# Kernel optimization log

Hardware: AMD Instinct MI355X
Metric: run time of the kernel (lower is better)

The kernel has to match this reference:

```python
import jax, jax.numpy as jnp
import numpy as np

B, L, K, E, D, H = 16, 512, 48, 128, 384, 128

def _gelu(x):
    return jax.nn.gelu(x, approximate=False)  # torch nn.GELU default is erf-based

def setup_inputs() -> dict:
    key = jax.random.key(0)
    ks = jax.random.split(key, 16)
    def randn(k, shape, scale=1.0):
        return jax.random.normal(k, shape, dtype=jnp.float32) * scale
    inp = {
        "h_V": randn(ks[0], (B, L, D)),
        "h_E": randn(ks[1], (B, L, K, E)),
        "mask": jnp.ones((B, L), dtype=jnp.float32),
        "fw1": randn(ks[2], (E, D), 1.0 / np.sqrt(E)),
        "fb1": randn(ks[3], (D,), 0.02),
        "fw2": randn(ks[4], (D, D), 1.0 / np.sqrt(D)),
        "fb2": randn(ks[5], (D,), 0.02),
        "hw1": randn(ks[6], (D, H), 1.0 / np.sqrt(D)),
        "hb1": randn(ks[7], (H,), 0.02),
        "hw2": randn(ks[8], (H, H // 2), 1.0 / np.sqrt(H)),
        "hb2": randn(ks[9], (H // 2,), 0.02),
        "hw3": randn(ks[10], (H // 2, 1), 1.0 / np.sqrt(H // 2)),
        "hb3": randn(ks[11], (1,), 0.02),
        "E_idx": jax.random.randint(ks[12], (B, L, K), 0, L),
    }
    return inp

def reference(h_V, h_E, mask, fw1, fb1, fw2, fb2, hw1, hb1, hw2, hb2, hw3, hb3, E_idx):
    # CFConv: edge-conditioned filters [B,L,K,D]
    W = _gelu(_gelu(h_E @ fw1 + fb1) @ fw2 + fb2)
    # gather_nodes: x_j[b,l,k,:] = h_V[b, E_idx[b,l,k], :]
    x_j = jax.vmap(lambda x, idx: x[idx])(h_V, E_idx)  # [B,L,K,D]
    h = jnp.sum(x_j * W, axis=2)  # weighted sum over neighbors -> [B,L,D]
    # mlp_head (dropout = identity at inference)
    h = _gelu(h @ hw1 + hb1)
    h = _gelu(h @ hw2 + hb2)
    dG = (h @ hw3 + hb3)[..., 0]  # [B,L]
    valid_length = jnp.clip(jnp.sum(mask, axis=1), 1.0, None)  # [B]
    return jnp.sum(dG * mask, axis=1) / jnp.sqrt(valid_length)  # [B]
```

## Files before the change

### kernel.cpp

```cpp
#include <hip/hip_runtime.h>
#include <hip/hip_bf16.h>
#include <math.h>

#define NB 16
#define NL 512
#define NK 48
#define NE 128
#define ND 384
#define NH 128

typedef __attribute__((ext_vector_type(8))) short short8;
typedef __attribute__((ext_vector_type(4))) float f32x4;

__device__ __forceinline__ float gelu_fast(float x) {
    float t = x * fmaf(x * x, -0.1029437f, -2.3022087f);
    float e = __builtin_amdgcn_exp2f(t);
    return x * __builtin_amdgcn_rcpf(1.0f + e);
}

__device__ __forceinline__ unsigned short f2bf(float x) {
    union { float f; unsigned u; } v; v.f = x;
    unsigned r = v.u + 0x7fffu + ((v.u >> 16) & 1u);
    return (unsigned short)(r >> 16);
}

__device__ __forceinline__ unsigned short f2bf_rhu(float x) {
    union { float f; unsigned u; } v; v.f = x;
    return (unsigned short)((v.u + 0x8000u) >> 16);
}

__device__ __forceinline__ unsigned pk_bf16(float a, float b) {
    union { float f; unsigned u; } ua, ub; ua.f = a; ub.f = b;
    return __builtin_amdgcn_perm(ua.u + 0x8000u, ub.u + 0x8000u, 0x07060302u);
}

__global__ void pack_weights(const float* __restrict__ fw1,
                             const float* __restrict__ fw2,
                             const float* __restrict__ hw1,
                             const float* __restrict__ hw2,
                             unsigned short* __restrict__ fw1p,
                             unsigned short* __restrict__ fw2p,
                             unsigned short* __restrict__ hw1p,
                             unsigned short* __restrict__ hw2p) {
    int tid = blockIdx.x * 256 + threadIdx.x;
    if (tid < NE * ND) {
        int k = tid / ND, n = tid % ND;
        int dst = (((k >> 5) * 24 + (n >> 4)) * 64 + ((k >> 3) & 3) * 16 + (n & 15)) * 8 + (k & 7);
        fw1p[dst] = f2bf(fw1[tid]);
    } else if (tid < NE * ND + ND * ND) {
        int i = tid - NE * ND;
        int k = i / ND, n = i % ND;
        int dst = (((k >> 5) * 24 + (n >> 4)) * 64 + ((k >> 3) & 3) * 16 + (n & 15)) * 8 + (k & 7);
        fw2p[dst] = f2bf(fw2[i]);
    } else if (tid < NE * ND + ND * ND + ND * NH) {
        int i = tid - (NE * ND + ND * ND);
        int k = i / NH, n = i % NH;
        int dst = (((k >> 5) * 8 + (n >> 4)) * 64 + ((k >> 3) & 3) * 16 + (n & 15)) * 8 + (k & 7);
        hw1p[dst] = f2bf(hw1[i]);
    } else if (tid < NE * ND + ND * ND + ND * NH + NH * (NH / 2)) {
        int i = tid - (NE * ND + ND * ND + ND * NH);
        int k = i / (NH / 2), n = i % (NH / 2);
        int dst = (((k >> 5) * 4 + (n >> 4)) * 64 + ((k >> 3) & 3) * 16 + (n & 15)) * 8 + (k & 7);
        hw2p[dst] = f2bf(hw2[i]);
    }
}

__global__ __launch_bounds__(256, 3) void cfconv_kernel(
    const float* __restrict__ h_V, const float* __restrict__ h_E,
    const float* __restrict__ fb1, const float* __restrict__ fb2,
    const unsigned short* __restrict__ fw1p,
    const unsigned short* __restrict__ fw2p,
    const int* __restrict__ E_idx, unsigned short* __restrict__ hbufB)
{
    __shared__ unsigned short Ea[48 * 136];
    __shared__ unsigned short T[48 * 392];
    __shared__ int rowoff_s[48];

    const int t = threadIdx.x;
    const int wave = t >> 6, lane = t & 63;
    const int quad = lane >> 4, l16 = lane & 15;
    const int bl = blockIdx.x;
    const int wn0 = wave * 96;

    if (t < 48)
        rowoff_s[t] = ((bl >> 9) * NL + E_idx[bl * NK + t]) * ND;

    {
        const float4* src = (const float4*)(h_E + (size_t)bl * (NK * NE));
        #pragma unroll
        for (int i = 0; i < 6; i++) {
            int v = i * 256 + t;
            float4 d = src[v];
            int r = v >> 5;
            int c = (v & 31) * 4;
            uint2 u;
            u.x = pk_bf16(d.y, d.x);
            u.y = pk_bf16(d.w, d.z);
            *(uint2*)&Ea[r * 136 + c] = u;
        }
    }
    __syncthreads();

    f32x4 acc[18];

    #pragma unroll
    for (int i = 0; i < 18; i++) acc[i] = (f32x4){0.f, 0.f, 0.f, 0.f};

    #pragma unroll
    for (int kt = 0; kt < 4; kt++) {
        short8 aw[6], be[3];
        #pragma unroll
        for (int mt = 0; mt < 6; mt++)
            aw[mt] = *(const short8*)(fw1p + (size_t)((kt * 24 + (wn0 >> 4) + mt) * 64 + lane) * 8);
        #pragma unroll
        for (int nt = 0; nt < 3; nt++)
            be[nt] = *(const short8*)&Ea[(nt * 16 + l16) * 136 + kt * 32 + quad * 8];
        #pragma unroll
        for (int mt = 0; mt < 6; mt++)
            #pragma unroll
            for (int nt = 0; nt < 3; nt++)
                acc[mt * 3 + nt] = __builtin_amdgcn_mfma_f32_16x16x32_bf16(
                    aw[mt], be[nt], acc[mt * 3 + nt], 0, 0, 0);
    }

    #pragma unroll
    for (int mt = 0; mt < 6; mt++) {
        float4 b1v = *(const float4*)&fb1[wn0 + mt * 16 + quad * 4];
        #pragma unroll
        for (int nt = 0; nt < 3; nt++) {
            f32x4 a = acc[mt * 3 + nt];
            float v0 = gelu_fast(a[0] + b1v.x);
            float v1 = gelu_fast(a[1] + b1v.y);
            float v2 = gelu_fast(a[2] + b1v.z);
            float v3 = gelu_fast(a[3] + b1v.w);
            uint2 u;
            u.x = pk_bf16(v1, v0);
            u.y = pk_bf16(v3, v2);
            *(uint2*)&T[(nt * 16 + l16) * 392 + wn0 + mt * 16 + quad * 4] = u;
        }
    }
    __syncthreads();

    #pragma unroll
    for (int i = 0; i < 18; i++) acc[i] = (f32x4){0.f, 0.f, 0.f, 0.f};

    {
        short8 b0[6], b1[6], af[3];
        #define LOADB(kt, bf)                                                            \
            _Pragma("unroll")                                                            \
            for (int nt = 0; nt < 6; nt++)                                               \
                bf[nt] = *(const short8*)(fw2p +                                         \
                    (size_t)(((kt) * 24 + (wn0 >> 4) + nt) * 64 + lane) * 8);
        #define LOADA(kt)                                                                \
            _Pragma("unroll")                                                            \
            for (int mt = 0; mt < 3; mt++)                                               \
                af[mt] = *(const short8*)&T[(mt * 16 + l16) * 392 + (kt) * 32 + quad * 8];
        #define MFMAS(bf)                                                                \
            _Pragma("unroll")                                                            \
            for (int mt = 0; mt < 3; mt++)                                               \
                _Pragma("unroll")                                                        \
                for (int nt = 0; nt < 6; nt++)                                           \
                    acc[nt * 3 + mt] = __builtin_amdgcn_mfma_f32_16x16x32_bf16(          \
                        af[mt], bf[nt], acc[nt * 3 + mt], 0, 0, 0);

        LOADB(0, b0);
        for (int kt = 0; kt < 10; kt += 2) {
            LOADB(kt + 1, b1);
            LOADA(kt);
            MFMAS(b0);
            LOADB(kt + 2, b0);
            LOADA(kt + 1);
            MFMAS(b1);
        }
        LOADB(11, b1);
        LOADA(10);
        MFMAS(b0);
        LOADA(11);
        MFMAS(b1);
        #undef LOADB
        #undef LOADA
        #undef MFMAS
    }

    float b2v[6];
    #pragma unroll
    for (int nt = 0; nt < 6; nt++) b2v[nt] = fb2[wn0 + nt * 16 + l16];

    float s[6] = {0.f, 0.f, 0.f, 0.f, 0.f, 0.f};
    #pragma unroll
    for (int mt = 0; mt < 3; mt++) {
        const int rb = mt * 16 + quad * 4;
        const float* p0 = h_V + rowoff_s[rb + 0] + wn0 + l16;
        const float* p1 = h_V + rowoff_s[rb + 1] + wn0 + l16;
        const float* p2 = h_V + rowoff_s[rb + 2] + wn0 + l16;
        const float* p3 = h_V + rowoff_s[rb + 3] + wn0 + l16;
        float xv[6][4];
        #pragma unroll
        for (int nt = 0; nt < 6; nt++) {
            xv[nt][0] = p0[nt * 16];
            xv[nt][1] = p1[nt * 16];
            xv[nt][2] = p2[nt * 16];
            xv[nt][3] = p3[nt * 16];
        }
        #pragma unroll
        for (int nt = 0; nt < 6; nt++)
            #pragma unroll
            for (int r = 0; r < 4; r++)
                s[nt] = fmaf(gelu_fast(acc[nt * 3 + mt][r] + b2v[nt]), xv[nt][r], s[nt]);
    }
    #pragma unroll
    for (int nt = 0; nt < 6; nt++) {
        float v = s[nt];
        v += __shfl_xor(v, 16, 64);
        v += __shfl_xor(v, 32, 64);
        if (lane < 16)
            hbufB[(size_t)bl * ND + wn0 + nt * 16 + lane] = f2bf(v);
    }
}

__global__ __launch_bounds__(64) void head_kernel(
    const unsigned short* __restrict__ hbufB,
    const unsigned short* __restrict__ hw1p, const float* __restrict__ hb1,
    const unsigned short* __restrict__ hw2p, const float* __restrict__ hb2,
    const float* __restrict__ hw3, const float* __restrict__ hb3,
    const float* __restrict__ mask, float* __restrict__ dGpart)
{
    __shared__ unsigned short T1[16 * 136];
    const int lane = threadIdx.x;
    const int quad = lane >> 4, l16 = lane & 15;
    const int row0 = blockIdx.x * 16;

    f32x4 acc1[8];
    #pragma unroll
    for (int nt = 0; nt < 8; nt++) acc1[nt] = (f32x4){0.f, 0.f, 0.f, 0.f};

    for (int kt = 0; kt < 12; kt++) {
        short8 a = *(const short8*)(hbufB + (size_t)(row0 + l16) * ND + kt * 32 + quad * 8);
        #pragma unroll
        for (int nt = 0; nt < 8; nt++) {
            short8 b = *(const short8*)(hw1p + (size_t)((kt * 8 + nt) * 64 + lane) * 8);
            acc1[nt] = __builtin_amdgcn_mfma_f32_16x16x32_bf16(a, b, acc1[nt], 0, 0, 0);
        }
    }

    #pragma unroll
    for (int nt = 0; nt < 8; nt++) {
        int col = nt * 16 + l16;
        float b1 = hb1[col];
        #pragma unroll
        for (int r = 0; r < 4; r++)
            T1[(quad * 4 + r) * 136 + col] = f2bf_rhu(gelu_fast(acc1[nt][r] + b1));
    }
    __syncthreads();

    f32x4 acc2[4];
    #pragma unroll
    for (int nt = 0; nt < 4; nt++) acc2[nt] = (f32x4){0.f, 0.f, 0.f, 0.f};

    #pragma unroll
    for (int kt = 0; kt < 4; kt++) {
        short8 a = *(const short8*)&T1[l16 * 136 + kt * 32 + quad * 8];
        #pragma unroll
        for (int nt = 0; nt < 4; nt++) {
            short8 b = *(const short8*)(hw2p + (size_t)((kt * 4 + nt) * 64 + lane) * 8);
            acc2[nt] = __builtin_amdgcn_mfma_f32_16x16x32_bf16(a, b, acc2[nt], 0, 0, 0);
        }
    }

    float w3[4], b2[4];
    #pragma unroll
    for (int nt = 0; nt < 4; nt++) { w3[nt] = hw3[nt * 16 + l16]; b2[nt] = hb2[nt * 16 + l16]; }

    float dsum = 0.f;
    const float hb3v = hb3[0];
    #pragma unroll
    for (int r = 0; r < 4; r++) {
        float pr = 0.f;
        #pragma unroll
        for (int nt = 0; nt < 4; nt++)
            pr = fmaf(gelu_fast(acc2[nt][r] + b2[nt]), w3[nt], pr);
        pr += __shfl_xor(pr, 1, 64);
        pr += __shfl_xor(pr, 2, 64);
        pr += __shfl_xor(pr, 4, 64);
        pr += __shfl_xor(pr, 8, 64);
        if (l16 == 0) {
            int grow = row0 + quad * 4 + r;
            dsum = fmaf(pr + hb3v, mask[grow], dsum);
        }
    }
    dsum += __shfl_xor(dsum, 16, 64);
    dsum += __shfl_xor(dsum, 32, 64);
    if (lane == 0) dGpart[blockIdx.x] = dsum;
}

__global__ void finalize_kernel(const float* __restrict__ dGpart,
                                const float* __restrict__ mask,
                                float* __restrict__ out) {
    int t = threadIdx.x;
    int b = t >> 4, j = t & 15;
    float ms = 0.f;
    for (int l = j; l < NL; l += 16) ms += mask[b * NL + l];
    float dg = dGpart[b * 32 + j] + dGpart[b * 32 + 16 + j];
    #pragma unroll
    for (int d = 1; d < 16; d <<= 1) {
        ms += __shfl_xor(ms, d, 64);
        dg += __shfl_xor(dg, d, 64);
    }
    if (j == 0) {
        ms = fmaxf(ms, 1.0f);
        out[b] = dg / sqrtf(ms);
    }
}

extern "C" void kernel_launch(void* const* d_in, const int* in_sizes, int n_in,
                              void* d_out, int out_size, void* d_ws, size_t ws_size,
                              hipStream_t stream) {
    const float* h_V  = (const float*)d_in[0];
    const float* h_E  = (const float*)d_in[1];
    const float* mask = (const float*)d_in[2];
    const float* fw1  = (const float*)d_in[3];
    const float* fb1  = (const float*)d_in[4];
    const float* fw2  = (const float*)d_in[5];
    const float* fb2  = (const float*)d_in[6];
    const float* hw1  = (const float*)d_in[7];
    const float* hb1  = (const float*)d_in[8];
    const float* hw2  = (const float*)d_in[9];
    const float* hb2  = (const float*)d_in[10];
    const float* hw3  = (const float*)d_in[11];
    const float* hb3  = (const float*)d_in[12];
    const int*   E_idx = (const int*)d_in[13];
    float* out = (float*)d_out;

    char* ws = (char*)d_ws;
    unsigned short* fw1p = (unsigned short*)ws;
    unsigned short* fw2p = (unsigned short*)(ws + 98304);
    unsigned short* hw1p = (unsigned short*)(ws + 393216);
    unsigned short* hw2p = (unsigned short*)(ws + 491520);
    float* dGpart = (float*)(ws + 507904);
    unsigned short* hbufB = (unsigned short*)(ws + 512000);

    pack_weights<<<992, 256, 0, stream>>>(fw1, fw2, hw1, hw2, fw1p, fw2p, hw1p, hw2p);
    cfconv_kernel<<<NB * NL, 256, 0, stream>>>(h_V, h_E, fb1, fb2, fw1p, fw2p, E_idx, hbufB);
    head_kernel<<<(NB * NL) / 16, 64, 0, stream>>>(hbufB, hw1p, hb1, hw2p, hb2, hw3, hb3, mask, dGpart);
    finalize_kernel<<<1, 256, 0, stream>>>(dGpart, mask, out);
}
```

Before: 453.8 us.

## Process four nodes per block with register prefetch of next node's edges

Each block of the CFConv kernel now loops over four consecutive (b,l) nodes instead of one. The next node's h_E tile and neighbor indices are loaded into registers while the current node's two GEMMs run, then written to shared memory at the end of the iteration. The second GEMM is split into two 48-column passes so fewer accumulators are live, which offsets the extra prefetch registers. The aim is to hide global load latency and amortize block launch cost. In exchange the grid has four times fewer blocks, which reduces parallelism across CUs, and extra barriers are added per node.

```diff
diff --git a/kernel.cpp b/kernel.cpp
--- a/kernel.cpp
+++ b/kernel.cpp
@@ -8,6 +8,7 @@
 #define NE 128
 #define ND 384
 #define NH 128
+#define GRP 4
 
 typedef __attribute__((ext_vector_type(8))) short short8;
 typedef __attribute__((ext_vector_type(4))) float f32x4;
@@ -74,147 +75,179 @@
 {
     __shared__ unsigned short Ea[48 * 136];
     __shared__ unsigned short T[48 * 392];
-    __shared__ int rowoff_s[48];
+    __shared__ int rowoff_s[2][48];
 
     const int t = threadIdx.x;
     const int wave = t >> 6, lane = t & 63;
     const int quad = lane >> 4, l16 = lane & 15;
-    const int bl = blockIdx.x;
+    const int bl0 = blockIdx.x * GRP;
     const int wn0 = wave * 96;
 
-    if (t < 48)
-        rowoff_s[t] = ((bl >> 9) * NL + E_idx[bl * NK + t]) * ND;
-
+    float4 st[6];
     {
-        const float4* src = (const float4*)(h_E + (size_t)bl * (NK * NE));
+        const float4* src = (const float4*)(h_E + (size_t)bl0 * (NK * NE));
+        #pragma unroll
+        for (int i = 0; i < 6; i++) st[i] = src[i * 256 + t];
+        if (t < 48)
+            rowoff_s[0][t] = ((bl0 >> 9) * NL + E_idx[bl0 * NK + t]) * ND;
         #pragma unroll
         for (int i = 0; i < 6; i++) {
             int v = i * 256 + t;
-            float4 d = src[v];
-            int r = v >> 5;
-            int c = (v & 31) * 4;
+            int r = v >> 5, c = (v & 31) * 4;
             uint2 u;
-            u.x = pk_bf16(d.y, d.x);
-            u.y = pk_bf16(d.w, d.z);
+            u.x = pk_bf16(st[i].y, st[i].x);
+            u.y = pk_bf16(st[i].w, st[i].z);
             *(uint2*)&Ea[r * 136 + c] = u;
         }
     }
     __syncthreads();
 
-    f32x4 acc[18];
-
-    #pragma unroll
-    for (int i = 0; i < 18; i++) acc[i] = (f32x4){0.f, 0.f, 0.f, 0.f};
-
-    #pragma unroll
-    for (int kt = 0; kt < 4; kt++) {
-        short8 aw[6], be[3];
-        #pragma unroll
-        for (int mt = 0; mt < 6; mt++)
-            aw[mt] = *(const short8*)(fw1p + (size_t)((kt * 24 + (wn0 >> 4) + mt) * 64 + lane) * 8);
-        #pragma unroll
-        for (int nt = 0; nt < 3; nt++)
-            be[nt] = *(const short8*)&Ea[(nt * 16 + l16) * 136 + kt * 32 + quad * 8];
-        #pragma unroll
-        for (int mt = 0; mt < 6; mt++)
+    for (int g = 0; g < GRP; g++) {
+        const int bl = bl0 + g;
+        const bool has_next = (g + 1 < GRP);
+
+        int nidx = 0;
+        if (has_next) {
+            const float4* srcn = (const float4*)(h_E + (size_t)(bl + 1) * (NK * NE));
+            #pragma unroll
+            for (int i = 0; i < 6; i++) st[i] = srcn[i * 256 + t];
+            if (t < 48) nidx = E_idx[(bl + 1) * NK + t];
+        }
+
+        f32x4 acc1[18];
+        #pragma unroll
+        for (int i = 0; i < 18; i++) acc1[i] = (f32x4){0.f, 0.f, 0.f, 0.f};
+
+        #pragma unroll
+        for (int kt = 0; kt < 4; kt++) {
+            short8 aw[6], be[3];
+            #pragma unroll
+            for (int mt = 0; mt < 6; mt++)
+                aw[mt] = *(const short8*)(fw1p + (size_t)((kt * 24 + (wn0 >> 4) + mt) * 64 + lane) * 8);
             #pragma unroll
             for (int nt = 0; nt < 3; nt++)
-                acc[mt * 3 + nt] = __builtin_amdgcn_mfma_f32_16x16x32_bf16(
-                    aw[mt], be[nt], acc[mt * 3 + nt], 0, 0, 0);
-    }
-
-    #pragma unroll
-    for (int mt = 0; mt < 6; mt++) {
-        float4 b1v = *(const float4*)&fb1[wn0 + mt * 16 + quad * 4];
-        #pragma unroll
-        for (int nt = 0; nt < 3; nt++) {
-            f32x4 a = acc[mt * 3 + nt];
-            float v0 = gelu_fast(a[0] + b1v.x);
-            float v1 = gelu_fast(a[1] + b1v.y);
-            float v2 = gelu_fast(a[2] + b1v.z);
-            float v3 = gelu_fast(a[3] + b1v.w);
-            uint2 u;
-            u.x = pk_bf16(v1, v0);
-            u.y = pk_bf16(v3, v2);
-            *(uint2*)&T[(nt * 16 + l16) * 392 + wn0 + mt * 16 + quad * 4] = u;
-        }
-    }
-    __syncthreads();
-
-    #pragma unroll
-    for (int i = 0; i < 18; i++) acc[i] = (f32x4){0.f, 0.f, 0.f, 0.f};
-
-    {
-        short8 b0[6], b1[6], af[3];
-        #define LOADB(kt, bf)                                                            \
-            _Pragma("unroll")                                                            \
-            for (int nt = 0; nt < 6; nt++)                                               \
-                bf[nt] = *(const short8*)(fw2p +                                         \
-                    (size_t)(((kt) * 24 + (wn0 >> 4) + nt) * 64 + lane) * 8);
-        #define LOADA(kt)                                                                \
-            _Pragma("unroll")                                                            \
-            for (int mt = 0; mt < 3; mt++)                                               \
-                af[mt] = *(const short8*)&T[(mt * 16 + l16) * 392 + (kt) * 32 + quad * 8];
-        #define MFMAS(bf)                                                                \
-            _Pragma("unroll")                                                            \
-            for (int mt = 0; mt < 3; mt++)                                               \
-                _Pragma("unroll")                                                        \
-                for (int nt = 0; nt < 6; nt++)                                           \
-                    acc[nt * 3 + mt] = __builtin_amdgcn_mfma_f32_16x16x32_bf16(          \
-                        af[mt], bf[nt], acc[nt * 3 + mt], 0, 0, 0);
-
-        LOADB(0, b0);
-        for (int kt = 0; kt < 10; kt += 2) {
-            LOADB(kt + 1, b1);
-            LOADA(kt);
-            MFMAS(b0);
-            LOADB(kt + 2, b0);
-            LOADA(kt + 1);
-            MFMAS(b1);
-        }
-        LOADB(11, b1);
-        LOADA(10);
-        MFMAS(b0);
-        LOADA(11);
-        MFMAS(b1);
-        #undef LOADB
-        #undef LOADA
-        #undef MFMAS
-    }
-
-    float b2v[6];
-    #pragma unroll
-    for (int nt = 0; nt < 6; nt++) b2v[nt] = fb2[wn0 + nt * 16 + l16];
-
-    float s[6] = {0.f, 0.f, 0.f, 0.f, 0.f, 0.f};
-    #pragma unroll
-    for (int mt = 0; mt < 3; mt++) {
-        const int rb = mt * 16 + quad * 4;
-        const float* p0 = h_V + rowoff_s[rb + 0] + wn0 + l16;
-        const float* p1 = h_V + rowoff_s[rb + 1] + wn0 + l16;
-        const float* p2 = h_V + rowoff_s[rb + 2] + wn0 + l16;
-        const float* p3 = h_V + rowoff_s[rb + 3] + wn0 + l16;
-        float xv[6][4];
-        #pragma unroll
-        for (int nt = 0; nt < 6; nt++) {
-            xv[nt][0] = p0[nt * 16];
-            xv[nt][1] = p1[nt * 16];
-            xv[nt][2] = p2[nt * 16];
-            xv[nt][3] = p3[nt * 16];
-        }
-        #pragma unroll
-        for (int nt = 0; nt < 6; nt++)
-            #pragma unroll
-            for (int r = 0; r < 4; r++)
-                s[nt] = fmaf(gelu_fast(acc[nt * 3 + mt][r] + b2v[nt]), xv[nt][r], s[nt]);
-    }
-    #pragma unroll
-    for (int nt = 0; nt < 6; nt++) {
-        float v = s[nt];
-        v += __shfl_xor(v, 16, 64);
-        v += __shfl_xor(v, 32, 64);
-        if (lane < 16)
-            hbufB[(size_t)bl * ND + wn0 + nt * 16 + lane] = f2bf(v);
+                be[nt] = *(const short8*)&Ea[(nt * 16 + l16) * 136 + kt * 32 + quad * 8];
+            #pragma unroll
+            for (int mt = 0; mt < 6; mt++)
+                #pragma unroll
+                for (int nt = 0; nt < 3; nt++)
+                    acc1[mt * 3 + nt] = __builtin_amdgcn_mfma_f32_16x16x32_bf16(
+                        aw[mt], be[nt], acc1[mt * 3 + nt], 0, 0, 0);
+        }
+
+        #pragma unroll
+        for (int mt = 0; mt < 6; mt++) {
+            float4 b1v = *(const float4*)&fb1[wn0 + mt * 16 + quad * 4];
+            #pragma unroll
+            for (int nt = 0; nt < 3; nt++) {
+                f32x4 a = acc1[mt * 3 + nt];
+                float v0 = gelu_fast(a[0] + b1v.x);
+                float v1 = gelu_fast(a[1] + b1v.y);
+                float v2 = gelu_fast(a[2] + b1v.z);
+                float v3 = gelu_fast(a[3] + b1v.w);
+                uint2 u;
+                u.x = pk_bf16(v1, v0);
+                u.y = pk_bf16(v3, v2);
+                *(uint2*)&T[(nt * 16 + l16) * 392 + wn0 + mt * 16 + quad * 4] = u;
+            }
+        }
+        __syncthreads();
+
+        #pragma unroll
+        for (int p = 0; p < 2; p++) {
+            const int cb = wn0 + p * 48;
+            f32x4 acc[9];
+            #pragma unroll
+            for (int i = 0; i < 9; i++) acc[i] = (f32x4){0.f, 0.f, 0.f, 0.f};
+
+            {
+                short8 b0[3], b1[3], af[3];
+                #define LOADB(kt, bf)                                                        \
+                    _Pragma("unroll")                                                        \
+                    for (int nt = 0; nt < 3; nt++)                                           \
+                        bf[nt] = *(const short8*)(fw2p +                                     \
+                            (size_t)(((kt) * 24 + (cb >> 4) + nt) * 64 + lane) * 8);
+                #define LOADA(kt)                                                            \
+                    _Pragma("unroll")                                                        \
+                    for (int mt = 0; mt < 3; mt++)                                           \
+                        af[mt] = *(const short8*)&T[(mt * 16 + l16) * 392 + (kt) * 32 + quad * 8];
+                #define MFMAS(bf)                                                            \
+                    _Pragma("unroll")                                                        \
+                    for (int mt = 0; mt < 3; mt++)                                           \
+                        _Pragma("unroll")                                                    \
+                        for (int nt = 0; nt < 3; nt++)                                       \
+                            acc[nt * 3 + mt] = __builtin_amdgcn_mfma_f32_16x16x32_bf16(      \
+                                af[mt], bf[nt], acc[nt * 3 + mt], 0, 0, 0);
+
+                LOADB(0, b0);
+                for (int kt = 0; kt < 10; kt += 2) {
+                    LOADB(kt + 1, b1);
+                    LOADA(kt);
+                    MFMAS(b0);
+                    LOADB(kt + 2, b0);
+                    LOADA(kt + 1);
+                    MFMAS(b1);
+                }
+                LOADB(11, b1);
+                LOADA(10);
+                MFMAS(b0);
+                LOADA(11);
+                MFMAS(b1);
+                #undef LOADB
+                #undef LOADA
+                #undef MFMAS
+            }
+
+            float b2v[3];
+            #pragma unroll
+            for (int nt = 0; nt < 3; nt++) b2v[nt] = fb2[cb + nt * 16 + l16];
+
+            float s[3] = {0.f, 0.f, 0.f};
+            #pragma unroll
+            for (int mt = 0; mt < 3; mt++) {
+                const int rb = mt * 16 + quad * 4;
+                const float* p0 = h_V + rowoff_s[g & 1][rb + 0] + cb + l16;
+                const float* p1 = h_V + rowoff_s[g & 1][rb + 1] + cb + l16;
+                const float* p2 = h_V + rowoff_s[g & 1][rb + 2] + cb + l16;
+                const float* p3 = h_V + rowoff_s[g & 1][rb + 3] + cb + l16;
+                float xv[3][4];
+                #pragma unroll
+                for (int nt = 0; nt < 3; nt++) {
+                    xv[nt][0] = p0[nt * 16];
+                    xv[nt][1] = p1[nt * 16];
+                    xv[nt][2] = p2[nt * 16];
+                    xv[nt][3] = p3[nt * 16];
+                }
+                #pragma unroll
+                for (int nt = 0; nt < 3; nt++)
+                    #pragma unroll
+                    for (int r = 0; r < 4; r++)
+                        s[nt] = fmaf(gelu_fast(acc[nt * 3 + mt][r] + b2v[nt]), xv[nt][r], s[nt]);
+            }
+            #pragma unroll
+            for (int nt = 0; nt < 3; nt++) {
+                float v = s[nt];
+                v += __shfl_xor(v, 16, 64);
+                v += __shfl_xor(v, 32, 64);
+                if (lane < 16)
+                    hbufB[(size_t)bl * ND + cb + nt * 16 + lane] = f2bf(v);
+            }
+        }
+
+        if (has_next) {
+            if (t < 48)
+                rowoff_s[(g + 1) & 1][t] = (((bl + 1) >> 9) * NL + nidx) * ND;
+            #pragma unroll
+            for (int i = 0; i < 6; i++) {
+                int v = i * 256 + t;
+                int r = v >> 5, c = (v & 31) * 4;
+                uint2 u;
+                u.x = pk_bf16(st[i].y, st[i].x);
+                u.y = pk_bf16(st[i].w, st[i].z);
+                *(uint2*)&Ea[r * 136 + c] = u;
+            }
+        }
+        __syncthreads();
     }
 }
 
@@ -340,7 +373,7 @@
     unsigned short* hbufB = (unsigned short*)(ws + 512000);
 
     pack_weights<<<992, 256, 0, stream>>>(fw1, fw2, hw1, hw2, fw1p, fw2p, hw1p, hw2p);
-    cfconv_kernel<<<NB * NL, 256, 0, stream>>>(h_V, h_E, fb1, fb2, fw1p, fw2p, E_idx, hbufB);
+    cfconv_kernel<<<(NB * NL) / GRP, 256, 0, stream>>>(h_V, h_E, fb1, fb2, fw1p, fw2p, E_idx, hbufB);
     head_kernel<<<(NB * NL) / 16, 64, 0, stream>>>(hbufB, hw1p, hb1, hw2p, hb2, hw3, hb3, mask, dGpart);
     finalize_kernel<<<1, 256, 0, stream>>>(dGpart, mask, out);
 }
```

New measurement: 1.296 ms. 2.86x slower.
